# Kernel optimization log

Hardware: AMD Instinct MI355X
Metric: run time of the kernel (lower is better)

The kernel has to match this reference:

```python
import jax, jax.numpy as jnp
import numpy as np

N_WIRES = 12
N_LAYERS = 3
DIM = 2 ** N_WIRES
BATCH = 512


def _rot_matrix(a, b, c):
    """Fused U = RZ(c) @ RY(b) @ RX(a) as a 2x2 complex64 matrix."""
    ca, sa = jnp.cos(a * 0.5), jnp.sin(a * 0.5)
    cb, sb = jnp.cos(b * 0.5), jnp.sin(b * 0.5)
    ec = jnp.exp(-0.5j * c)  # e^{-i c/2}
    zero = jnp.zeros_like(ec)
    RX = jnp.stack([jnp.stack([ca + 0j, -1j * sa]),
                    jnp.stack([-1j * sa, ca + 0j])]).astype(jnp.complex64)
    RY = jnp.stack([jnp.stack([cb, -sb]),
                    jnp.stack([sb, cb])]).astype(jnp.complex64)
    RZ = jnp.stack([jnp.stack([ec, zero]),
                    jnp.stack([zero, jnp.conj(ec)])]).astype(jnp.complex64)
    return RZ @ RY @ RX


def _apply_1q(psi, U, wire):
    B = psi.shape[0]
    dl, dr = 2 ** wire, 2 ** (N_WIRES - wire - 1)
    s = psi.reshape(B, dl, 2, dr)
    s = jnp.einsum('ij,bljr->blir', U, s)
    return s.reshape(B, DIM)


def _apply_cnot_adjacent(psi, wire):
    # CNOT(control=wire, target=wire+1): permute (10 <-> 11) on the joint axis
    B = psi.shape[0]
    dl, dr = 2 ** wire, 2 ** (N_WIRES - wire - 2)
    s = psi.reshape(B, dl, 4, dr)
    s = jnp.take(s, jnp.array([0, 1, 3, 2]), axis=2)
    return s.reshape(B, DIM)


def _circuit(state_batch, weights):
    psi = state_batch.astype(jnp.complex64)  # QubitStateVector init
    for l in range(N_LAYERS):
        for w in range(N_WIRES):
            U = _rot_matrix(weights[l, w, 0], weights[l, w, 1], weights[l, w, 2])
            psi = _apply_1q(psi, U, w)
        for w in range(N_WIRES - 1):  # 'cnot' chain entanglement
            psi = _apply_cnot_adjacent(psi, w)
    B = state_batch.shape[0]
    probs = (psi.real ** 2 + psi.imag ** 2).reshape((B,) + (2,) * N_WIRES)
    feats = []
    for w in range(N_WIRES):  # <Z_w> = p(0) - p(1)
        axes = tuple(a for a in range(1, N_WIRES + 1) if a != w + 1)
        p = probs.sum(axis=axes)  # (B, 2)
        feats.append(p[:, 0] - p[:, 1])
    return jnp.stack(feats, axis=-1)  # (B, N_WIRES)


def setup_inputs() -> dict:
    key = jax.random.key(0)
    k1, k2, k3, k4 = jax.random.split(key, 4)
    state = jax.random.normal(k1, (BATCH, DIM), dtype=jnp.float32)
    state = state / jnp.linalg.norm(state, axis=-1, keepdims=True)  # valid quantum states
    weights = jax.random.uniform(k2, (N_LAYERS, N_WIRES, 3), dtype=jnp.float32,
                                 minval=0.0, maxval=2.0 * np.pi)
    head_w = jax.random.normal(k3, (1, N_WIRES), dtype=jnp.float32) / np.sqrt(N_WIRES)
    head_b = jax.random.normal(k4, (1,), dtype=jnp.float32) * 0.01
    return {"state_batch": state, "weights": weights, "head_w": head_w, "head_b": head_b}


def reference(state_batch, weights, head_w, head_b):
    feats = _circuit(state_batch, weights)          # (B, N_WIRES) PauliZ expvals
    out = feats @ head_w.T + head_b                 # Linear(num_wires, 1)
    return out[:, 0]                                # squeeze(-1) -> (B,)
```

## Files before the change

kernel.cpp:

```cpp
#include <hip/hip_runtime.h>


namespace {

constexpr int N_WIRES  = 12;
constexpr int DIM      = 1 << N_WIRES;
constexpr int N_LAYERS = 3;
constexpr int THREADS  = 256;
constexpr int PER      = DIM / THREADS;
constexpr int NGATES   = N_LAYERS * N_WIRES;
constexpr int PADDED   = DIM + (DIM >> 4);

__device__ __forceinline__ void apply4(float ar[PER], float ai[PER],
                                       const float (*Um)[8], int gbase)
{
    #pragma unroll
    for (int gg = 0; gg < 4; ++gg) {
        const float4 uA = *reinterpret_cast<const float4*>(&Um[gbase + gg][0]);
        const float4 uB = *reinterpret_cast<const float4*>(&Um[gbase + gg][4]);
        const float u00r = uA.x, u00i = uA.y, u01r = uA.z, u01i = uA.w;
        const float u10r = uB.x, u10i = uB.y, u11r = uB.z, u11i = uB.w;
        const int st = 8 >> gg;
        #pragma unroll
        for (int k0 = 0; k0 < PER; ++k0) {
            if (k0 & st) continue;
            const int k1 = k0 | st;
            const float r0 = ar[k0], m0 = ai[k0];
            const float r1 = ar[k1], m1 = ai[k1];
            ar[k0] = u00r * r0 - u00i * m0 + u01r * r1 - u01i * m1;
            ai[k0] = u00r * m0 + u00i * r0 + u01r * m1 + u01i * r1;
            ar[k1] = u10r * r0 - u10i * m0 + u11r * r1 - u11i * m1;
            ai[k1] = u10r * m0 + u10i * r0 + u11r * m1 + u11i * r1;
        }
    }
}

__global__ __launch_bounds__(THREADS, 2)
void qcirc_kernel(const float* __restrict__ state,
                  const float* __restrict__ weights,
                  const float* __restrict__ head_w,
                  const float* __restrict__ head_b,
                  float* __restrict__ out)
{
    __shared__ float2 buf[PADDED];
    __shared__ __align__(16) float Umat[NGATES][8];
    __shared__ float redbuf[THREADS / 64];

    const int tid = threadIdx.x;
    const int b   = blockIdx.x;

    if (tid < NGATES) {
        const float* wp = weights + tid * 3;
        float ha = 0.5f * wp[0], hb = 0.5f * wp[1], hc = 0.5f * wp[2];
        float ca = cosf(ha), sa = sinf(ha);
        float cb = cosf(hb), sb = sinf(hb);
        float ecr = cosf(hc), eci = -sinf(hc);
        float t0 = cb * ca, t1 = sb * sa, t2 = sb * ca, t3 = cb * sa;
        float u00r =  ecr * t0 - eci * t1;
        float u00i =  ecr * t1 + eci * t0;
        float u10r =  ecr * t2 - eci * t3;
        float u10i = -ecr * t3 - eci * t2;
        Umat[tid][0] =  u00r;  Umat[tid][1] =  u00i;
        Umat[tid][2] = -u10r;  Umat[tid][3] =  u10i;
        Umat[tid][4] =  u10r;  Umat[tid][5] =  u10i;
        Umat[tid][6] =  u00r;  Umat[tid][7] = -u00i;
    }

    float ar[PER], ai[PER];
    {
        const float* sp = state + (size_t)b * DIM;
        #pragma unroll
        for (int k = 0; k < PER; ++k) {
            ar[k] = sp[(k << 8) | tid];
            ai[k] = 0.f;
        }
    }
    __syncthreads();

    #pragma unroll 1
    for (int l = 0; l < N_LAYERS; ++l) {
        if (l > 0) {
            #pragma unroll
            for (int k = 0; k < PER; ++k) {
                int i = (k << 8) | tid;
                int j = i ^ (i >> 1);
                float2 v = buf[j + (j >> 4)];
                ar[k] = v.x; ai[k] = v.y;
            }
            __syncthreads();
        }

        apply4(ar, ai, Umat, l * 12 + 0);
        #pragma unroll
        for (int k = 0; k < PER; ++k) {
            int i = (k << 8) | tid;
            buf[i + (i >> 4)] = make_float2(ar[k], ai[k]);
        }
        __syncthreads();

        #pragma unroll
        for (int k = 0; k < PER; ++k) {
            int i = ((tid & 0xF0) << 4) | (k << 4) | (tid & 15);
            float2 v = buf[i + (i >> 4)];
            ar[k] = v.x; ai[k] = v.y;
        }
        apply4(ar, ai, Umat, l * 12 + 4);
        #pragma unroll
        for (int k = 0; k < PER; ++k) {
            int i = ((tid & 0xF0) << 4) | (k << 4) | (tid & 15);
            buf[i + (i >> 4)] = make_float2(ar[k], ai[k]);
        }
        __syncthreads();

        #pragma unroll
        for (int k = 0; k < PER; ++k) {
            int i = (tid << 4) | k;
            float2 v = buf[i + (i >> 4)];
            ar[k] = v.x; ai[k] = v.y;
        }
        apply4(ar, ai, Umat, l * 12 + 8);
        if (l < N_LAYERS - 1) {
            #pragma unroll
            for (int k = 0; k < PER; ++k) {
                int i = (tid << 4) | k;
                buf[i + (i >> 4)] = make_float2(ar[k], ai[k]);
            }
            __syncthreads();
        }
    }

    float hw[N_WIRES];
    #pragma unroll
    for (int w = 0; w < N_WIRES; ++w) hw[w] = head_w[w];

    int it = tid ^ (tid >> 1); it ^= it >> 2; it ^= it >> 4;
    float chi = 0.f;
    #pragma unroll
    for (int w = 0; w < 8; ++w)
        chi += ((it >> (7 - w)) & 1) ? -hw[w] : hw[w];
    const int parfill = (__popc(tid) & 1) ? 0xF : 0;

    float acc = 0.f;
    #pragma unroll
    for (int k = 0; k < PER; ++k) {
        int ml = k ^ (k >> 1); ml ^= ml >> 2; ml ^= parfill;
        float c = chi;
        #pragma unroll
        for (int w = 8; w < 12; ++w)
            c += ((ml >> (11 - w)) & 1) ? -hw[w] : hw[w];
        float p = ar[k] * ar[k] + ai[k] * ai[k];
        acc += p * c;
    }

    #pragma unroll
    for (int off = 32; off > 0; off >>= 1)
        acc += __shfl_down(acc, off, 64);
    if ((tid & 63) == 0) redbuf[tid >> 6] = acc;
    __syncthreads();
    if (tid == 0) {
        float s = 0.f;
        #pragma unroll
        for (int q = 0; q < THREADS / 64; ++q) s += redbuf[q];
        out[b] = s + head_b[0];
    }
}

}

extern "C" void kernel_launch(void* const* d_in, const int* in_sizes, int n_in,
                              void* d_out, int out_size, void* d_ws, size_t ws_size,
                              hipStream_t stream)
{
    const float* state   = (const float*)d_in[0];
    const float* weights = (const float*)d_in[1];
    const float* head_w  = (const float*)d_in[2];
    const float* head_b  = (const float*)d_in[3];
    float* out = (float*)d_out;

    const int batch = in_sizes[0] / DIM;
    qcirc_kernel<<<batch, THREADS, 0, stream>>>(state, weights, head_w, head_b, out);
}
```

Before: 87.18 us.

## Use 512 threads per state with 8 amplitudes each and four shared-memory passes

Each batch block now runs 512 threads, each holding 8 amplitudes instead of 16. Every layer is split into four register-resident stages of 3 gates each, connected by shared-memory transposes, where before it was three stages of 4 gates. The aim is more parallelism and latency hiding per state and lower register pressure. In exchange each layer does an extra shared-memory round trip and an extra barrier, and the final Z-expectation parity index math is adjusted to match.

```diff
diff --git a/kernel.cpp b/kernel.cpp
--- a/kernel.cpp
+++ b/kernel.cpp
@@ -6,21 +6,23 @@
 constexpr int N_WIRES  = 12;
 constexpr int DIM      = 1 << N_WIRES;
 constexpr int N_LAYERS = 3;
-constexpr int THREADS  = 256;
+constexpr int THREADS  = 512;
 constexpr int PER      = DIM / THREADS;
 constexpr int NGATES   = N_LAYERS * N_WIRES;
 constexpr int PADDED   = DIM + (DIM >> 4);
 
-__device__ __forceinline__ void apply4(float ar[PER], float ai[PER],
+__device__ __forceinline__ int pad(int i) { return i + (i >> 4); }
+
+__device__ __forceinline__ void apply3(float ar[PER], float ai[PER],
                                        const float (*Um)[8], int gbase)
 {
     #pragma unroll
-    for (int gg = 0; gg < 4; ++gg) {
+    for (int gg = 0; gg < 3; ++gg) {
         const float4 uA = *reinterpret_cast<const float4*>(&Um[gbase + gg][0]);
         const float4 uB = *reinterpret_cast<const float4*>(&Um[gbase + gg][4]);
         const float u00r = uA.x, u00i = uA.y, u01r = uA.z, u01i = uA.w;
         const float u10r = uB.x, u10i = uB.y, u11r = uB.z, u11i = uB.w;
-        const int st = 8 >> gg;
+        const int st = 4 >> gg;
         #pragma unroll
         for (int k0 = 0; k0 < PER; ++k0) {
             if (k0 & st) continue;
@@ -35,7 +37,7 @@
     }
 }
 
-__global__ __launch_bounds__(THREADS, 2)
+__global__ __launch_bounds__(THREADS, 4)
 void qcirc_kernel(const float* __restrict__ state,
                   const float* __restrict__ weights,
                   const float* __restrict__ head_w,
@@ -46,11 +48,11 @@
     __shared__ __align__(16) float Umat[NGATES][8];
     __shared__ float redbuf[THREADS / 64];
 
-    const int tid = threadIdx.x;
-    const int b   = blockIdx.x;
+    const int t = threadIdx.x;
+    const int b = blockIdx.x;
 
-    if (tid < NGATES) {
-        const float* wp = weights + tid * 3;
+    if (t < NGATES) {
+        const float* wp = weights + t * 3;
         float ha = 0.5f * wp[0], hb = 0.5f * wp[1], hc = 0.5f * wp[2];
         float ca = cosf(ha), sa = sinf(ha);
         float cb = cosf(hb), sb = sinf(hb);
@@ -60,10 +62,10 @@
         float u00i =  ecr * t1 + eci * t0;
         float u10r =  ecr * t2 - eci * t3;
         float u10i = -ecr * t3 - eci * t2;
-        Umat[tid][0] =  u00r;  Umat[tid][1] =  u00i;
-        Umat[tid][2] = -u10r;  Umat[tid][3] =  u10i;
-        Umat[tid][4] =  u10r;  Umat[tid][5] =  u10i;
-        Umat[tid][6] =  u00r;  Umat[tid][7] = -u00i;
+        Umat[t][0] =  u00r;  Umat[t][1] =  u00i;
+        Umat[t][2] = -u10r;  Umat[t][3] =  u10i;
+        Umat[t][4] =  u10r;  Umat[t][5] =  u10i;
+        Umat[t][6] =  u00r;  Umat[t][7] = -u00i;
     }
 
     float ar[PER], ai[PER];
@@ -71,7 +73,7 @@
         const float* sp = state + (size_t)b * DIM;
         #pragma unroll
         for (int k = 0; k < PER; ++k) {
-            ar[k] = sp[(k << 8) | tid];
+            ar[k] = sp[(k << 9) | t];
             ai[k] = 0.f;
         }
     }
@@ -79,51 +81,66 @@
 
     #pragma unroll 1
     for (int l = 0; l < N_LAYERS; ++l) {
+        const int gb = l * 12;
         if (l > 0) {
             #pragma unroll
             for (int k = 0; k < PER; ++k) {
-                int i = (k << 8) | tid;
+                int i = (k << 9) | t;
                 int j = i ^ (i >> 1);
-                float2 v = buf[j + (j >> 4)];
+                float2 v = buf[pad(j)];
                 ar[k] = v.x; ai[k] = v.y;
             }
             __syncthreads();
         }
 
-        apply4(ar, ai, Umat, l * 12 + 0);
+        apply3(ar, ai, Umat, gb + 0);
         #pragma unroll
         for (int k = 0; k < PER; ++k) {
-            int i = (k << 8) | tid;
-            buf[i + (i >> 4)] = make_float2(ar[k], ai[k]);
+            int i = (k << 9) | t;
+            buf[pad(i)] = make_float2(ar[k], ai[k]);
         }
         __syncthreads();
 
         #pragma unroll
         for (int k = 0; k < PER; ++k) {
-            int i = ((tid & 0xF0) << 4) | (k << 4) | (tid & 15);
-            float2 v = buf[i + (i >> 4)];
+            int i = ((t >> 6) << 9) | (k << 6) | (t & 63);
+            float2 v = buf[pad(i)];
             ar[k] = v.x; ai[k] = v.y;
         }
-        apply4(ar, ai, Umat, l * 12 + 4);
+        apply3(ar, ai, Umat, gb + 3);
         #pragma unroll
         for (int k = 0; k < PER; ++k) {
-            int i = ((tid & 0xF0) << 4) | (k << 4) | (tid & 15);
-            buf[i + (i >> 4)] = make_float2(ar[k], ai[k]);
+            int i = ((t >> 6) << 9) | (k << 6) | (t & 63);
+            buf[pad(i)] = make_float2(ar[k], ai[k]);
         }
         __syncthreads();
 
         #pragma unroll
         for (int k = 0; k < PER; ++k) {
-            int i = (tid << 4) | k;
-            float2 v = buf[i + (i >> 4)];
+            int i = ((t >> 3) << 6) | (k << 3) | (t & 7);
+            float2 v = buf[pad(i)];
             ar[k] = v.x; ai[k] = v.y;
         }
-        apply4(ar, ai, Umat, l * 12 + 8);
+        apply3(ar, ai, Umat, gb + 6);
+        #pragma unroll
+        for (int k = 0; k < PER; ++k) {
+            int i = ((t >> 3) << 6) | (k << 3) | (t & 7);
+            buf[pad(i)] = make_float2(ar[k], ai[k]);
+        }
+        __syncthreads();
+
+        #pragma unroll
+        for (int k = 0; k < PER; ++k) {
+            int i = (t << 3) | k;
+            float2 v = buf[pad(i)];
+            ar[k] = v.x; ai[k] = v.y;
+        }
+        apply3(ar, ai, Umat, gb + 9);
         if (l < N_LAYERS - 1) {
             #pragma unroll
             for (int k = 0; k < PER; ++k) {
-                int i = (tid << 4) | k;
-                buf[i + (i >> 4)] = make_float2(ar[k], ai[k]);
+                int i = (t << 3) | k;
+                buf[pad(i)] = make_float2(ar[k], ai[k]);
             }
             __syncthreads();
         }
@@ -133,21 +150,21 @@
     #pragma unroll
     for (int w = 0; w < N_WIRES; ++w) hw[w] = head_w[w];
 
-    int it = tid ^ (tid >> 1); it ^= it >> 2; it ^= it >> 4;
+    int it = t ^ (t >> 1); it ^= it >> 2; it ^= it >> 4; it ^= it >> 8;
     float chi = 0.f;
     #pragma unroll
-    for (int w = 0; w < 8; ++w)
-        chi += ((it >> (7 - w)) & 1) ? -hw[w] : hw[w];
-    const int parfill = (__popc(tid) & 1) ? 0xF : 0;
+    for (int w = 0; w < 9; ++w)
+        chi += ((it >> (8 - w)) & 1) ? -hw[w] : hw[w];
+    const int parfill = (__popc(t) & 1) ? 7 : 0;
 
     float acc = 0.f;
     #pragma unroll
     for (int k = 0; k < PER; ++k) {
-        int ml = k ^ (k >> 1); ml ^= ml >> 2; ml ^= parfill;
+        int ml = (k ^ (k >> 1) ^ (k >> 2)) ^ parfill;
         float c = chi;
-        #pragma unroll
-        for (int w = 8; w < 12; ++w)
-            c += ((ml >> (11 - w)) & 1) ? -hw[w] : hw[w];
+        c += ((ml >> 2) & 1) ? -hw[9]  : hw[9];
+        c += ((ml >> 1) & 1) ? -hw[10] : hw[10];
+        c += ( ml       & 1) ? -hw[11] : hw[11];
         float p = ar[k] * ar[k] + ai[k] * ai[k];
         acc += p * c;
     }
@@ -155,9 +172,9 @@
     #pragma unroll
     for (int off = 32; off > 0; off >>= 1)
         acc += __shfl_down(acc, off, 64);
-    if ((tid & 63) == 0) redbuf[tid >> 6] = acc;
+    if ((t & 63) == 0) redbuf[t >> 6] = acc;
     __syncthreads();
-    if (tid == 0) {
+    if (t == 0) {
         float s = 0.f;
         #pragma unroll
         for (int q = 0; q < THREADS / 64; ++q) s += redbuf[q];
```

After: 87.91 us. Within noise of the previous version (+0.8%).

## Double-buffer shared state with stride-18 padding and packed float2 gate math

Applied to the files above, without the earlier changes.

Replaces the single padded shared buffer with two ping-pong buffers laid out with stride 18 per 16-element row. This lets some barriers be dropped and the contiguous phase use float4 shared-memory accesses. It also rewrites the gate update on float2 amplitudes with a J-rotation form, so the compiler can emit packed FMA instructions, and fully unrolls the layer loop. The cost is roughly doubled shared memory per block, which may lower occupancy, plus more complex index arithmetic.

```diff
diff --git a/kernel.cpp b/kernel.cpp
--- a/kernel.cpp
+++ b/kernel.cpp
@@ -5,32 +5,46 @@
 
 constexpr int N_WIRES  = 12;
 constexpr int DIM      = 1 << N_WIRES;
-constexpr int N_LAYERS = 3;
 constexpr int THREADS  = 256;
-constexpr int PER      = DIM / THREADS;
-constexpr int NGATES   = N_LAYERS * N_WIRES;
-constexpr int PADDED   = DIM + (DIM >> 4);
-
-__device__ __forceinline__ void apply4(float ar[PER], float ai[PER],
-                                       const float (*Um)[8], int gbase)
+constexpr int PER      = 16;
+constexpr int NGATES   = 36;
+constexpr int PADC     = 4606;
+
+__device__ __forceinline__ float2 axpy(float s, float2 v, float2 a) {
+    float2 sv = make_float2(s, s);
+    return make_float2(sv.x * v.x + a.x, sv.y * v.y + a.y);
+}
+__device__ __forceinline__ float2 scal(float s, float2 v) {
+    return make_float2(s * v.x, s * v.y);
+}
+__device__ __forceinline__ float2 Jrot(float2 v) { return make_float2(-v.y, v.x); }
+
+__device__ __forceinline__ void apply4(float2 amp[PER],
+                                       const float2 (*Um)[4], int gbase)
 {
     #pragma unroll
     for (int gg = 0; gg < 4; ++gg) {
-        const float4 uA = *reinterpret_cast<const float4*>(&Um[gbase + gg][0]);
-        const float4 uB = *reinterpret_cast<const float4*>(&Um[gbase + gg][4]);
-        const float u00r = uA.x, u00i = uA.y, u01r = uA.z, u01i = uA.w;
-        const float u10r = uB.x, u10i = uB.y, u11r = uB.z, u11i = uB.w;
+        const float2 u00 = Um[gbase + gg][0];
+        const float2 u01 = Um[gbase + gg][1];
+        const float2 u10 = Um[gbase + gg][2];
+        const float2 u11 = Um[gbase + gg][3];
         const int st = 8 >> gg;
         #pragma unroll
         for (int k0 = 0; k0 < PER; ++k0) {
             if (k0 & st) continue;
             const int k1 = k0 | st;
-            const float r0 = ar[k0], m0 = ai[k0];
-            const float r1 = ar[k1], m1 = ai[k1];
-            ar[k0] = u00r * r0 - u00i * m0 + u01r * r1 - u01i * m1;
-            ai[k0] = u00r * m0 + u00i * r0 + u01r * m1 + u01i * r1;
-            ar[k1] = u10r * r0 - u10i * m0 + u11r * r1 - u11i * m1;
-            ai[k1] = u10r * m0 + u10i * r0 + u11r * m1 + u11i * r1;
+            const float2 p = amp[k0], q = amp[k1];
+            const float2 jp = Jrot(p), jq = Jrot(q);
+            float2 np = scal(u00.x, p);
+            np = axpy(u00.y, jp, np);
+            np = axpy(u01.x, q,  np);
+            np = axpy(u01.y, jq, np);
+            float2 nq = scal(u10.x, p);
+            nq = axpy(u10.y, jp, nq);
+            nq = axpy(u11.x, q,  nq);
+            nq = axpy(u11.y, jq, nq);
+            amp[k0] = np;
+            amp[k1] = nq;
         }
     }
 }
@@ -42,15 +56,15 @@
                   const float* __restrict__ head_b,
                   float* __restrict__ out)
 {
-    __shared__ float2 buf[PADDED];
-    __shared__ __align__(16) float Umat[NGATES][8];
+    __shared__ __align__(16) float2 buf[2][PADC];
+    __shared__ __align__(16) float2 Umat[NGATES][4];
     __shared__ float redbuf[THREADS / 64];
 
-    const int tid = threadIdx.x;
-    const int b   = blockIdx.x;
-
-    if (tid < NGATES) {
-        const float* wp = weights + tid * 3;
+    const int t = threadIdx.x;
+    const int b = blockIdx.x;
+
+    if (t < NGATES) {
+        const float* wp = weights + t * 3;
         float ha = 0.5f * wp[0], hb = 0.5f * wp[1], hc = 0.5f * wp[2];
         float ca = cosf(ha), sa = sinf(ha);
         float cb = cosf(hb), sb = sinf(hb);
@@ -60,104 +74,113 @@
         float u00i =  ecr * t1 + eci * t0;
         float u10r =  ecr * t2 - eci * t3;
         float u10i = -ecr * t3 - eci * t2;
-        Umat[tid][0] =  u00r;  Umat[tid][1] =  u00i;
-        Umat[tid][2] = -u10r;  Umat[tid][3] =  u10i;
-        Umat[tid][4] =  u10r;  Umat[tid][5] =  u10i;
-        Umat[tid][6] =  u00r;  Umat[tid][7] = -u00i;
-    }
-
-    float ar[PER], ai[PER];
+        Umat[t][0] = make_float2( u00r,  u00i);
+        Umat[t][1] = make_float2(-u10r,  u10i);
+        Umat[t][2] = make_float2( u10r,  u10i);
+        Umat[t][3] = make_float2( u00r, -u00i);
+    }
+
+    const int T  = t >> 4, u = t & 15;
+    const int bA = 18 * T + u;
+    const int bB = 288 * T + 18 * 0 + u;
+    const int bC = 18 * t;
+    const int tb  = t ^ (t >> 1);
+    const int tbx = tb ^ 128;
+    const int pb0 = 18 * (tb  >> 4) + (tb  & 15);
+    const int pb1 = 18 * (tbx >> 4) + (tbx & 15);
+
+    float2 amp[PER];
     {
         const float* sp = state + (size_t)b * DIM;
         #pragma unroll
-        for (int k = 0; k < PER; ++k) {
-            ar[k] = sp[(k << 8) | tid];
-            ai[k] = 0.f;
-        }
+        for (int k = 0; k < PER; ++k)
+            amp[k] = make_float2(sp[(k << 8) | t], 0.f);
     }
     __syncthreads();
 
-    #pragma unroll 1
-    for (int l = 0; l < N_LAYERS; ++l) {
+    #pragma unroll
+    for (int l = 0; l < 3; ++l) {
+        const int gb = l * 12;
         if (l > 0) {
+            const float2* src = buf[(3 * l - 1) & 1];
             #pragma unroll
             for (int k = 0; k < PER; ++k) {
-                int i = (k << 8) | tid;
-                int j = i ^ (i >> 1);
-                float2 v = buf[j + (j >> 4)];
-                ar[k] = v.x; ai[k] = v.y;
+                const int g = k ^ (k >> 1);
+                amp[k] = src[((k & 1) ? pb1 : pb0) + 288 * g];
             }
+        }
+
+        apply4(amp, Umat, gb + 0);
+        {
+            float2* w = &buf[(3 * l) & 1][bA];
+            #pragma unroll
+            for (int k = 0; k < PER; ++k) w[288 * k] = amp[k];
+        }
+        __syncthreads();
+        {
+            const float2* r = &buf[(3 * l) & 1][bB];
+            #pragma unroll
+            for (int k = 0; k < PER; ++k) amp[k] = r[18 * k];
+        }
+
+        apply4(amp, Umat, gb + 4);
+        {
+            float2* w = &buf[(3 * l + 1) & 1][bB];
+            #pragma unroll
+            for (int k = 0; k < PER; ++k) w[18 * k] = amp[k];
+        }
+        __syncthreads();
+        {
+            const float4* r = reinterpret_cast<const float4*>(&buf[(3 * l + 1) & 1][bC]);
+            #pragma unroll
+            for (int k = 0; k < PER / 2; ++k) {
+                float4 v = r[k];
+                amp[2 * k]     = make_float2(v.x, v.y);
+                amp[2 * k + 1] = make_float2(v.z, v.w);
+            }
+        }
+
+        apply4(amp, Umat, gb + 8);
+        if (l < 2) {
+            float4* w = reinterpret_cast<float4*>(&buf[(3 * l + 2) & 1][bC]);
+            #pragma unroll
+            for (int k = 0; k < PER / 2; ++k)
+                w[k] = make_float4(amp[2 * k].x, amp[2 * k].y,
+                                   amp[2 * k + 1].x, amp[2 * k + 1].y);
             __syncthreads();
         }
-
-        apply4(ar, ai, Umat, l * 12 + 0);
-        #pragma unroll
-        for (int k = 0; k < PER; ++k) {
-            int i = (k << 8) | tid;
-            buf[i + (i >> 4)] = make_float2(ar[k], ai[k]);
-        }
-        __syncthreads();
-
-        #pragma unroll
-        for (int k = 0; k < PER; ++k) {
-            int i = ((tid & 0xF0) << 4) | (k << 4) | (tid & 15);
-            float2 v = buf[i + (i >> 4)];
-            ar[k] = v.x; ai[k] = v.y;
-        }
-        apply4(ar, ai, Umat, l * 12 + 4);
-        #pragma unroll
-        for (int k = 0; k < PER; ++k) {
-            int i = ((tid & 0xF0) << 4) | (k << 4) | (tid & 15);
-            buf[i + (i >> 4)] = make_float2(ar[k], ai[k]);
-        }
-        __syncthreads();
-
-        #pragma unroll
-        for (int k = 0; k < PER; ++k) {
-            int i = (tid << 4) | k;
-            float2 v = buf[i + (i >> 4)];
-            ar[k] = v.x; ai[k] = v.y;
-        }
-        apply4(ar, ai, Umat, l * 12 + 8);
-        if (l < N_LAYERS - 1) {
-            #pragma unroll
-            for (int k = 0; k < PER; ++k) {
-                int i = (tid << 4) | k;
-                buf[i + (i >> 4)] = make_float2(ar[k], ai[k]);
-            }
-            __syncthreads();
-        }
     }
 
     float hw[N_WIRES];
     #pragma unroll
     for (int w = 0; w < N_WIRES; ++w) hw[w] = head_w[w];
 
-    int it = tid ^ (tid >> 1); it ^= it >> 2; it ^= it >> 4;
+    int it = t ^ (t >> 1); it ^= it >> 2; it ^= it >> 4;
     float chi = 0.f;
     #pragma unroll
     for (int w = 0; w < 8; ++w)
         chi += ((it >> (7 - w)) & 1) ? -hw[w] : hw[w];
-    const int parfill = (__popc(tid) & 1) ? 0xF : 0;
+    const int parfill = (__popc(t) & 1) ? 0xF : 0;
 
     float acc = 0.f;
     #pragma unroll
     for (int k = 0; k < PER; ++k) {
-        int ml = k ^ (k >> 1); ml ^= ml >> 2; ml ^= parfill;
+        int ml = (k ^ (k >> 1)); ml ^= ml >> 2; ml ^= parfill;
         float c = chi;
-        #pragma unroll
-        for (int w = 8; w < 12; ++w)
-            c += ((ml >> (11 - w)) & 1) ? -hw[w] : hw[w];
-        float p = ar[k] * ar[k] + ai[k] * ai[k];
+        c += ((ml >> 3) & 1) ? -hw[8]  : hw[8];
+        c += ((ml >> 2) & 1) ? -hw[9]  : hw[9];
+        c += ((ml >> 1) & 1) ? -hw[10] : hw[10];
+        c += ( ml       & 1) ? -hw[11] : hw[11];
+        float p = amp[k].x * amp[k].x + amp[k].y * amp[k].y;
         acc += p * c;
     }
 
     #pragma unroll
     for (int off = 32; off > 0; off >>= 1)
         acc += __shfl_down(acc, off, 64);
-    if ((tid & 63) == 0) redbuf[tid >> 6] = acc;
+    if ((t & 63) == 0) redbuf[t >> 6] = acc;
     __syncthreads();
-    if (tid == 0) {
+    if (t == 0) {
         float s = 0.f;
         #pragma unroll
         for (int q = 0; q < THREADS / 64; ++q) s += redbuf[q];
```

After: 84.58 us. 3.0% less time.
